# Optimization experiments

Hardware: AMD Instinct MI355X
Metric: run time of the kernel (lower is better)

The kernel has to match this reference:

```python
import jax, jax.numpy as jnp
import numpy as np
from jax import lax

CUTOFF = 0.25
SIGMA = 1.0
RADIUS = 4  # skimage/scipy default truncate=4.0 -> radius = round(4.0*sigma)


def _gauss_kernel(sigma=SIGMA, radius=RADIUS):
    x = np.arange(-radius, radius + 1, dtype=np.float32)
    k = np.exp(-0.5 * (x / sigma) ** 2)
    return jnp.asarray(k / k.sum())


def _blur_axis(x, axis, kernel):
    r = (kernel.shape[0] - 1) // 2
    pad = [(0, 0)] * x.ndim
    pad[axis] = (r, r)
    xp = jnp.pad(x, pad, mode='edge')  # scipy mode='nearest'
    out = jnp.zeros_like(x)
    for i in range(kernel.shape[0]):  # fixed small tap loop (9 taps)
        out = out + kernel[i] * lax.slice_in_dim(xp, i, i + x.shape[axis], axis=axis)
    return out


def gaussian_smoothing_4d(x):
    # skimage.filters.gaussian on a 4D array smooths over ALL axes (B, C, H, W)
    k = _gauss_kernel().astype(x.dtype)
    for ax in range(4):
        x = _blur_axis(x, ax, k)
    return x


def dht_2d(x):
    # real(FFT(x)) - imag(FFT(flip(x)))
    return (jnp.fft.fftn(x, axes=(2, 3)).real
            - jnp.fft.fftn(jnp.flip(x, axis=(2, 3)), axes=(2, 3)).imag).astype(x.dtype)


def _neg_k(a):
    # X_H(-k): flip both spatial mode axes, then roll by 1 (DC stays put)
    return jnp.roll(jnp.flip(a, axis=(-2, -1)), shift=(1, 1), axis=(-2, -1))


def compl_mul2d(x1, x2):
    x1n, x2n = _neg_k(x1), _neg_k(x2)
    e = lambda a, b: jnp.einsum('bixy,ioxy->boxy', a, b)
    return 0.5 * (e(x1, x2) - e(x1n, x2n) + e(x1, x2n) + e(x1n, x2))


def setup_inputs() -> dict:
    key = jax.random.key(0)
    k1, k2 = jax.random.split(key)
    B, Cin, Cout, H, W, M1, M2 = 16, 64, 64, 128, 128, 20, 20
    x = jax.random.normal(k1, (B, Cin, H, W), dtype=jnp.float32)
    scale = 1.0 / (Cin * Cout)
    w1 = scale * jax.random.uniform(k2, (Cin, Cout, M1, M2), dtype=jnp.float32)
    return {'x': x, 'w1': w1}


def reference(x, w1):
    B, _, H, W = x.shape
    Cout, M1, M2 = w1.shape[1], w1.shape[2], w1.shape[3]
    x_ht = dht_2d(x)
    out_ht = jnp.zeros((B, Cout, H, W), dtype=x.dtype)
    out_ht = out_ht.at[:, :, :M1, :M2].set(
        compl_mul2d(x_ht[:, :, :M1, :M2], w1))
    # inverse DHT = DHT / (H*W)
    y = dht_2d(out_ht) / (H * W)
    y = gaussian_smoothing_4d(y)
    # low-pass mask along last dim only (as in the original)
    freqs = jnp.fft.fftfreq(W)
    mask = (jnp.abs(freqs) <= CUTOFF).astype(y.dtype)
    return y * mask
```

## Files before the change

### kernel.cpp

```cpp
#include <hip/hip_runtime.h>


#define TWO_PI 6.283185307179586f
#define THETA (TWO_PI / 128.0f)

__device__ __forceinline__ void gauss9(float* g) {
  float s = 0.f;
#pragma unroll
  for (int t = 0; t < 9; ++t) { float d = (float)(t - 4); g[t] = expf(-0.5f * d * d); s += g[t]; }
  float inv = 1.f / s;
#pragma unroll
  for (int t = 0; t < 9; ++t) g[t] *= inv;
}

__global__ void kA_init(float* __restrict__ L2g, float* __restrict__ RB2g,
                        float* __restrict__ Tg, float* __restrict__ Lf2g,
                        const float* __restrict__ w1, float* __restrict__ wbT) {
  __shared__ float sh[5632];
  int tid = threadIdx.x;
  int blk = blockIdx.x;
  if (blk == 1) {
    for (int i = tid; i < 5120; i += 256) {
      int n2 = i / 40, col = i - n2 * 40;
      int k2 = (col < 20) ? col : col - 20;
      float a = (float)((k2 * n2) & 127) * THETA;
      Tg[i] = (col < 20) ? cosf(a) : sinf(a);
    }
    return;
  }
  if (blk == 2) {
    for (int i = tid; i < 10240; i += 256) {
      int k1 = i >> 9, t = i & 511;
      int q = t >> 7, n1 = t & 127;
      int nn = n1 + ((q >= 2) ? 1 : 0);
      float a = (float)((k1 * nn) & 127) * THETA;
      float v;
      if (q == 0) v = cosf(a);
      else if (q == 1) v = -sinf(a);
      else if (q == 2) v = -sinf(a);
      else v = -cosf(a);
      Lf2g[i] = v;
    }
    return;
  }
  if (blk == 0) {
    for (int i = tid; i < 5376; i += 256) {
      int u = i / 42, t = i - u * 42;
      int A = (t < 21) ? t : t - 21;
      float a = (float)((u * A) & 127) * THETA;
      sh[u * 44 + t] = (t < 21) ? cosf(a) : sinf(a);
    }
    __syncthreads();
    float g[9]; gauss9(g);
    for (int i = tid; i < 5376; i += 256) {
      int u = i / 42, t = i - u * 42;
      float acc = 0.f;
#pragma unroll
      for (int tp = 0; tp < 9; ++tp) {
        int uc = u - 4 + tp; uc = uc < 0 ? 0 : (uc > 127 ? 127 : uc);
        acc += g[tp] * sh[uc * 44 + t];
      }
      L2g[t * 128 + u] = acc;
      bool keep = (u <= 32) || (u >= 96);
      RB2g[t * 128 + u] = keep ? acc : 0.f;
    }
    return;
  }
  int bb = blk - 3;
  int c = bb / 7, chunk = bb % 7;
  int m0 = chunk * 64;
  int mw = 400 - m0; if (mw > 64) mw = 64;
  for (int t = tid; t < 4096; t += 256) {
    int o = t >> 6, mm = t & 63;
    sh[o * 69 + mm] = (mm < mw) ? w1[(c * 64 + o) * 400 + m0 + mm] : 0.f;
  }
  __syncthreads();
  float g[9]; gauss9(g);
  for (int t = tid; t < 4096; t += 256) {
    int mm = t >> 6, o = t & 63;
    if (mm >= mw) continue;
    float acc = 0.f;
#pragma unroll
    for (int tp = 0; tp < 9; ++tp) {
      int oc = o - 4 + tp; oc = oc < 0 ? 0 : (oc > 63 ? 63 : oc);
      acc += g[tp] * sh[oc * 69 + mm];
    }
    wbT[(c * 400 + m0 + mm) * 64 + o] = acc;
  }
}

__global__ void __launch_bounds__(256, 4) k12(const float* __restrict__ x,
                                              const float* __restrict__ Tg,
                                              const float* __restrict__ Lf2g,
                                              float* __restrict__ X1) {
  __shared__ float lds[10240];
  int bc = blockIdx.x, tid = threadIdx.x;
  const float* xb = x + (long)bc * 16384;

  for (int t = tid; t < 5120; t += 256) lds[t] = Tg[t];

  int rg = tid & 31, cg = tid >> 5;
  int r0 = rg * 4, c0 = cg * 5;
  float acc[4][5];
#pragma unroll
  for (int i = 0; i < 4; ++i)
#pragma unroll
    for (int j = 0; j < 5; ++j) acc[i][j] = 0.f;

  float* xs = lds + 5120;
  for (int ch = 0; ch < 4; ++ch) {
    __syncthreads();
    for (int t = tid; t < 1024; t += 256) {
      int n2l = t & 31, n1g = t >> 5;
      const float* gp = xb + n1g * 512 + ch * 32 + n2l;
      float4 v = make_float4(gp[0], gp[128], gp[256], gp[384]);
      *(float4*)&xs[n2l * 132 + n1g * 4] = v;
    }
    __syncthreads();
#pragma unroll 4
    for (int k = 0; k < 32; ++k) {
      float4 av = *(const float4*)&xs[k * 132 + r0];
      const float* tr = lds + (ch * 32 + k) * 40 + c0;
      float avv[4] = {av.x, av.y, av.z, av.w};
      float bvv[5] = {tr[0], tr[1], tr[2], tr[3], tr[4]};
#pragma unroll
      for (int i = 0; i < 4; ++i)
#pragma unroll
        for (int j = 0; j < 5; ++j) acc[i][j] += avv[i] * bvv[j];
    }
  }
  __syncthreads();
#pragma unroll
  for (int j = 0; j < 5; ++j) {
    int col = c0 + j;
    int k2 = (col < 20) ? col : col - 20;
    int part = (col < 20) ? 0 : 128;
    int m = ((k2 >> 1) & 7) << 2;
    float* row = lds + k2 * 512;
    *(float4*)&row[(part + r0) ^ m] =
        make_float4(acc[0][j], acc[1][j], acc[2][j], acc[3][j]);
  }
  __syncthreads();
  for (int t = tid; t < 2560; t += 256) {
    int k2 = t >> 7, n1 = t & 127;
    int m = ((k2 >> 1) & 7) << 2;
    float* row = lds + k2 * 512;
    float pc = row[n1 ^ m], ps = row[(128 + n1) ^ m];
    float ck, sk;
    sincosf(THETA * (float)k2, &sk, &ck);
    row[(256 + n1) ^ m] = ck * pc - sk * ps;
    row[(384 + n1) ^ m] = sk * pc + ck * ps;
  }
  __syncthreads();
  if (tid < 200) {
    int k1 = tid / 10, k2 = (tid % 10) * 2;
    int m = ((k2 >> 1) & 7) << 2;
    const float* p0r = lds + k2 * 512;
    const float* p1r = lds + (k2 + 1) * 512;
    const float* lrow = Lf2g + k1 * 512;
    float a0 = 0.f, a1 = 0.f;
    for (int t = 0; t < 512; t += 4) {
      float4 l = *(const float4*)(lrow + t);
      int ts = t ^ m;
      float4 p0 = *(const float4*)(p0r + ts);
      float4 p1 = *(const float4*)(p1r + ts);
      a0 += l.x * p0.x + l.y * p0.y + l.z * p0.z + l.w * p0.w;
      a1 += l.x * p1.x + l.y * p1.y + l.z * p1.z + l.w * p1.w;
    }
    X1[(k1 * 20 + k2) * 1024 + bc] = a0;
    X1[(k1 * 20 + k2 + 1) * 1024 + bc] = a1;
  }
}

__global__ void k3_mix(const float* __restrict__ X1, const float* __restrict__ wbT,
                       float* __restrict__ O) {
  __shared__ float Xp[4][64], Xm[4][64];
  int m = blockIdx.x >> 2, bq = blockIdx.x & 3;
  int i = m / 20, j = m - i * 20;
  int nm = ((20 - i) % 20) * 20 + ((20 - j) % 20);
  int tid = threadIdx.x;
  const float sc = 0.5f / 16384.0f;
  float g[9]; gauss9(g);
  {
    int bl = tid >> 6, c = tid & 63;
    int b = bq * 4 + bl;
    float sa = 0.f, sn = 0.f;
#pragma unroll
    for (int tp = 0; tp < 9; ++tp) {
      int bb = b - 4 + tp; bb = bb < 0 ? 0 : (bb > 15 ? 15 : bb);
      sa += g[tp] * X1[m * 1024 + bb * 64 + c];
      sn += g[tp] * X1[nm * 1024 + bb * 64 + c];
    }
    Xp[bl][c] = (sa + sn) * sc; Xm[bl][c] = (sa - sn) * sc;
  }
  __syncthreads();
  int o = tid & 63, bl = tid >> 6;
  int b = bq * 4 + bl;
  float acc = 0.f;
#pragma unroll 4
  for (int c = 0; c < 64; ++c) {
    acc += wbT[(c * 400 + m) * 64 + o] * Xp[bl][c]
         + wbT[(c * 400 + nm) * 64 + o] * Xm[bl][c];
  }
  O[(b * 64 + o) * 400 + m] = acc;
}

__global__ void __launch_bounds__(256) k5b_final(const float* __restrict__ O,
                                                 const float* __restrict__ L2g,
                                                 const float* __restrict__ RB2g,
                                                 float* __restrict__ out) {
  __shared__ float Os[400];
  __shared__ float Rs[42 * 128];
  int bo = blockIdx.x, tid = threadIdx.x;
  for (int t = tid; t < 400; t += 256) Os[t] = O[bo * 400 + t];
  __syncthreads();
  const float4* Bc4 = (const float4*)RB2g;
  const float4* Bs4 = (const float4*)(RB2g + 21 * 128);
  {
    int vq = tid & 31, rg = tid >> 5;
    if (rg < 7) {
      int r0 = rg * 6;
      float4 a[6];
#pragma unroll
      for (int i = 0; i < 6; ++i) a[i] = make_float4(0.f, 0.f, 0.f, 0.f);
      for (int k2 = 0; k2 <= 20; ++k2) {
        float4 bc = Bc4[k2 * 32 + vq];
        float4 bs = Bs4[k2 * 32 + vq];
#pragma unroll
        for (int i = 0; i < 6; ++i) {
          int r = r0 + i;
          bool isS = (r >= 21);
          int A = isS ? (r - 21) : r;
          if (k2 < 20 && A < 20) {
            float ov = Os[A * 20 + k2];
            const float4 b = isS ? bs : bc;
            float s = isS ? -ov : ov;
            a[i].x += s * b.x; a[i].y += s * b.y; a[i].z += s * b.z; a[i].w += s * b.w;
          }
          if (k2 >= 1 && A >= 1) {
            float ov = Os[(A - 1) * 20 + (k2 - 1)];
            const float4 b = isS ? bc : bs;
            a[i].x -= ov * b.x; a[i].y -= ov * b.y; a[i].z -= ov * b.z; a[i].w -= ov * b.w;
          }
        }
      }
#pragma unroll
      for (int i = 0; i < 6; ++i)
        *(float4*)&Rs[(r0 + i) * 128 + vq * 4] = a[i];
    }
  }
  __syncthreads();
  int ug = tid >> 4, vg = tid & 15;
  int u0 = ug * 8, v0 = vg * 4;
  float acc[8][8];
#pragma unroll
  for (int i = 0; i < 8; ++i)
#pragma unroll
    for (int j = 0; j < 8; ++j) acc[i][j] = 0.f;
  for (int r = 0; r < 42; ++r) {
    float4 a0 = *(const float4*)(L2g + r * 128 + u0);
    float4 a1 = *(const float4*)(L2g + r * 128 + u0 + 4);
    float4 b0 = *(const float4*)&Rs[r * 128 + v0];
    float4 b1 = *(const float4*)&Rs[r * 128 + 64 + v0];
    float av[8] = {a0.x, a0.y, a0.z, a0.w, a1.x, a1.y, a1.z, a1.w};
    float bv[8] = {b0.x, b0.y, b0.z, b0.w, b1.x, b1.y, b1.z, b1.w};
#pragma unroll
    for (int i = 0; i < 8; ++i)
#pragma unroll
      for (int j = 0; j < 8; ++j) acc[i][j] += av[i] * bv[j];
  }
  long base = (long)bo * 16384;
#pragma unroll
  for (int i = 0; i < 8; ++i) {
    float4 s0 = make_float4(acc[i][0], acc[i][1], acc[i][2], acc[i][3]);
    float4 s1 = make_float4(acc[i][4], acc[i][5], acc[i][6], acc[i][7]);
    *(float4*)&out[base + (u0 + i) * 128 + v0] = s0;
    *(float4*)&out[base + (u0 + i) * 128 + 64 + v0] = s1;
  }
}

extern "C" void kernel_launch(void* const* d_in, const int* in_sizes, int n_in,
                              void* d_out, int out_size, void* d_ws, size_t ws_size,
                              hipStream_t stream) {
  const float* x = (const float*)d_in[0];
  const float* w1 = (const float*)d_in[1];
  float* out = (float*)d_out;
  float* ws = (float*)d_ws;

  float* X1 = ws;
  float* O = X1 + 409600;
  float* wbT = O + 409600;
  float* Tg = wbT + 1638400;
  float* Lf2g = Tg + 5120;
  float* L2g = Lf2g + 10240;
  float* RB2g = L2g + 5376;

  hipLaunchKernelGGL(kA_init, dim3(451), dim3(256), 0, stream,
                     L2g, RB2g, Tg, Lf2g, w1, wbT);
  hipLaunchKernelGGL(k12, dim3(1024), dim3(256), 0, stream, x, Tg, Lf2g, X1);
  hipLaunchKernelGGL(k3_mix, dim3(1600), dim3(256), 0, stream, X1, wbT, O);
  hipLaunchKernelGGL(k5b_final, dim3(1024), dim3(256), 0, stream, O, L2g, RB2g, out);
}
```

Baseline: 200.5 us.

## Restructure k12 to halve LDS, read Tg from global, fold twiddle into final dot

The forward-transform kernel now uses 5 waves of 320 threads. Each wave owns 8 output columns and reads the Tg matrix straight from global/cache with uniform addresses instead of staging it in LDS, which halves shared memory and raises the occupancy target. The separate twiddle-rotation pass over LDS is removed: the rotation by cos/sin is folded algebraically into the final reduction, which now accumulates six partial dot products per output. This trades fewer LDS passes and syncs for more registers and more global/scalar loads of Tg and Lf2g.

```diff
diff --git a/kernel.cpp b/kernel.cpp
--- a/kernel.cpp
+++ b/kernel.cpp
@@ -89,86 +89,92 @@
   }
 }
 
-__global__ void __launch_bounds__(256, 4) k12(const float* __restrict__ x,
+__global__ void __launch_bounds__(320, 6) k12(const float* __restrict__ x,
                                               const float* __restrict__ Tg,
                                               const float* __restrict__ Lf2g,
                                               float* __restrict__ X1) {
-  __shared__ float lds[10240];
+  __shared__ float lds[5120];
   int bc = blockIdx.x, tid = threadIdx.x;
+  int w = __builtin_amdgcn_readfirstlane(tid >> 6);
+  int L = tid & 63;
   const float* xb = x + (long)bc * 16384;
-
-  for (int t = tid; t < 5120; t += 256) lds[t] = Tg[t];
-
-  int rg = tid & 31, cg = tid >> 5;
-  int r0 = rg * 4, c0 = cg * 5;
-  float acc[4][5];
-#pragma unroll
-  for (int i = 0; i < 4; ++i)
-#pragma unroll
-    for (int j = 0; j < 5; ++j) acc[i][j] = 0.f;
-
-  float* xs = lds + 5120;
+  const float* tgw = Tg + w * 8;
+
+  float acc[2][8];
+#pragma unroll
+  for (int i = 0; i < 2; ++i)
+#pragma unroll
+    for (int j = 0; j < 8; ++j) acc[i][j] = 0.f;
+
   for (int ch = 0; ch < 4; ++ch) {
     __syncthreads();
-    for (int t = tid; t < 1024; t += 256) {
+    for (int t = tid; t < 1024; t += 320) {
       int n2l = t & 31, n1g = t >> 5;
       const float* gp = xb + n1g * 512 + ch * 32 + n2l;
       float4 v = make_float4(gp[0], gp[128], gp[256], gp[384]);
-      *(float4*)&xs[n2l * 132 + n1g * 4] = v;
+      *(float4*)&lds[n2l * 132 + n1g * 4] = v;
     }
     __syncthreads();
 #pragma unroll 4
     for (int k = 0; k < 32; ++k) {
-      float4 av = *(const float4*)&xs[k * 132 + r0];
-      const float* tr = lds + (ch * 32 + k) * 40 + c0;
-      float avv[4] = {av.x, av.y, av.z, av.w};
-      float bvv[5] = {tr[0], tr[1], tr[2], tr[3], tr[4]};
-#pragma unroll
-      for (int i = 0; i < 4; ++i)
-#pragma unroll
-        for (int j = 0; j < 5; ++j) acc[i][j] += avv[i] * bvv[j];
-    }
-  }
-  __syncthreads();
-#pragma unroll
-  for (int j = 0; j < 5; ++j) {
-    int col = c0 + j;
+      float2 av = *(const float2*)&lds[k * 132 + 2 * L];
+      const float* tr = tgw + (ch * 32 + k) * 40;
+      float4 b0 = *(const float4*)tr;
+      float4 b1 = *(const float4*)(tr + 4);
+      float bv[8] = {b0.x, b0.y, b0.z, b0.w, b1.x, b1.y, b1.z, b1.w};
+#pragma unroll
+      for (int j = 0; j < 8; ++j) {
+        acc[0][j] += av.x * bv[j];
+        acc[1][j] += av.y * bv[j];
+      }
+    }
+  }
+  __syncthreads();
+#pragma unroll
+  for (int j = 0; j < 8; ++j) {
+    int col = w * 8 + j;
     int k2 = (col < 20) ? col : col - 20;
     int part = (col < 20) ? 0 : 128;
-    int m = ((k2 >> 1) & 7) << 2;
-    float* row = lds + k2 * 512;
-    *(float4*)&row[(part + r0) ^ m] =
-        make_float4(acc[0][j], acc[1][j], acc[2][j], acc[3][j]);
-  }
-  __syncthreads();
-  for (int t = tid; t < 2560; t += 256) {
-    int k2 = t >> 7, n1 = t & 127;
-    int m = ((k2 >> 1) & 7) << 2;
-    float* row = lds + k2 * 512;
-    float pc = row[n1 ^ m], ps = row[(128 + n1) ^ m];
-    float ck, sk;
-    sincosf(THETA * (float)k2, &sk, &ck);
-    row[(256 + n1) ^ m] = ck * pc - sk * ps;
-    row[(384 + n1) ^ m] = sk * pc + ck * ps;
+    int m = (k2 & 7) << 2;
+    *(float2*)&lds[k2 * 256 + ((part + 2 * L) ^ m)] =
+        make_float2(acc[0][j], acc[1][j]);
   }
   __syncthreads();
   if (tid < 200) {
     int k1 = tid / 10, k2 = (tid % 10) * 2;
-    int m = ((k2 >> 1) & 7) << 2;
-    const float* p0r = lds + k2 * 512;
-    const float* p1r = lds + (k2 + 1) * 512;
+    int m0 = (k2 & 7) << 2, m1 = ((k2 + 1) & 7) << 2;
     const float* lrow = Lf2g + k1 * 512;
-    float a0 = 0.f, a1 = 0.f;
-    for (int t = 0; t < 512; t += 4) {
-      float4 l = *(const float4*)(lrow + t);
-      int ts = t ^ m;
-      float4 p0 = *(const float4*)(p0r + ts);
-      float4 p1 = *(const float4*)(p1r + ts);
-      a0 += l.x * p0.x + l.y * p0.y + l.z * p0.z + l.w * p0.w;
-      a1 += l.x * p1.x + l.y * p1.y + l.z * p1.z + l.w * p1.w;
-    }
-    X1[(k1 * 20 + k2) * 1024 + bc] = a0;
-    X1[(k1 * 20 + k2 + 1) * 1024 + bc] = a1;
+    const float* p0 = lds + k2 * 256;
+    const float* p1 = lds + (k2 + 1) * 256;
+    float d0a = 0.f, d1a = 0.f, d2ca = 0.f, d2sa = 0.f, d3ca = 0.f, d3sa = 0.f;
+    float d0b = 0.f, d1b = 0.f, d2cb = 0.f, d2sb = 0.f, d3cb = 0.f, d3sb = 0.f;
+    for (int t = 0; t < 128; t += 4) {
+      float4 l0 = *(const float4*)(lrow + t);
+      float4 l1 = *(const float4*)(lrow + 128 + t);
+      float4 l2 = *(const float4*)(lrow + 256 + t);
+      float4 l3 = *(const float4*)(lrow + 384 + t);
+      float4 pc0 = *(const float4*)(p0 + (t ^ m0));
+      float4 ps0 = *(const float4*)(p0 + ((128 + t) ^ m0));
+      float4 pc1 = *(const float4*)(p1 + (t ^ m1));
+      float4 ps1 = *(const float4*)(p1 + ((128 + t) ^ m1));
+      d0a += l0.x*pc0.x + l0.y*pc0.y + l0.z*pc0.z + l0.w*pc0.w;
+      d1a += l1.x*ps0.x + l1.y*ps0.y + l1.z*ps0.z + l1.w*ps0.w;
+      d2ca += l2.x*pc0.x + l2.y*pc0.y + l2.z*pc0.z + l2.w*pc0.w;
+      d2sa += l2.x*ps0.x + l2.y*ps0.y + l2.z*ps0.z + l2.w*ps0.w;
+      d3ca += l3.x*pc0.x + l3.y*pc0.y + l3.z*pc0.z + l3.w*pc0.w;
+      d3sa += l3.x*ps0.x + l3.y*ps0.y + l3.z*ps0.z + l3.w*ps0.w;
+      d0b += l0.x*pc1.x + l0.y*pc1.y + l0.z*pc1.z + l0.w*pc1.w;
+      d1b += l1.x*ps1.x + l1.y*ps1.y + l1.z*ps1.z + l1.w*ps1.w;
+      d2cb += l2.x*pc1.x + l2.y*pc1.y + l2.z*pc1.z + l2.w*pc1.w;
+      d2sb += l2.x*ps1.x + l2.y*ps1.y + l2.z*ps1.z + l2.w*ps1.w;
+      d3cb += l3.x*pc1.x + l3.y*pc1.y + l3.z*pc1.z + l3.w*pc1.w;
+      d3sb += l3.x*ps1.x + l3.y*ps1.y + l3.z*ps1.z + l3.w*ps1.w;
+    }
+    float ska, cka, skb, ckb;
+    sincosf(THETA * (float)k2, &ska, &cka);
+    sincosf(THETA * (float)(k2 + 1), &skb, &ckb);
+    X1[(k1 * 20 + k2) * 1024 + bc] = d0a + d1a + cka * (d2ca + d3sa) + ska * (d3ca - d2sa);
+    X1[(k1 * 20 + k2 + 1) * 1024 + bc] = d0b + d1b + ckb * (d2cb + d3sb) + skb * (d3cb - d2sb);
   }
 }
 
@@ -297,7 +303,7 @@
 
   hipLaunchKernelGGL(kA_init, dim3(451), dim3(256), 0, stream,
                      L2g, RB2g, Tg, Lf2g, w1, wbT);
-  hipLaunchKernelGGL(k12, dim3(1024), dim3(256), 0, stream, x, Tg, Lf2g, X1);
+  hipLaunchKernelGGL(k12, dim3(1024), dim3(320), 0, stream, x, Tg, Lf2g, X1);
   hipLaunchKernelGGL(k3_mix, dim3(1600), dim3(256), 0, stream, X1, wbT, O);
   hipLaunchKernelGGL(k5b_final, dim3(1024), dim3(256), 0, stream, O, L2g, RB2g, out);
 }
```

Result: no change. 197.1 us (-1.7%).
